# Kernel optimization log

Hardware: AMD Instinct MI355X
Metric: run time of the kernel (lower is better)

## Reference

```python
import jax, jax.numpy as jnp
import numpy as np

B, DAYS, N, E = 2, 8, 10000, 80000
C_IN, C_OUT, H = 32, 32, 4
NEG_SLOPE = 0.2


def setup_inputs() -> dict:
    key = jax.random.key(0)
    ks = jax.random.split(key, 7)
    x = jax.random.randint(ks[0], (B, DAYS, N), 0, N)
    adjacency = jax.random.randint(ks[1], (2, E), 0, N)
    embedding = jax.random.normal(ks[2], (N, C_IN), dtype=jnp.float32)
    # GATConv linear: in_channels -> heads*out_channels
    W = jax.random.normal(ks[3], (C_IN, H * C_OUT), dtype=jnp.float32) / np.sqrt(C_IN)
    att_src = jax.random.normal(ks[4], (H, C_OUT), dtype=jnp.float32) / np.sqrt(C_OUT)
    att_dst = jax.random.normal(ks[5], (H, C_OUT), dtype=jnp.float32) / np.sqrt(C_OUT)
    bias = jnp.zeros((H * C_OUT,), dtype=jnp.float32)
    return {"x": x, "adjacency": adjacency, "embedding": embedding,
            "W": W, "att_src": att_src, "att_dst": att_dst, "bias": bias}


def _gat_forward(feat, src, dst, W, att_src, att_dst, bias):
    # feat: [G, N, C_IN]; same edge list shared across the G graphs
    G = feat.shape[0]
    xh = (feat @ W).reshape(G, N, H, C_OUT)              # [G,N,H,C]
    a_src = jnp.einsum('gnhc,hc->gnh', xh, att_src)       # [G,N,H]
    a_dst = jnp.einsum('gnhc,hc->gnh', xh, att_dst)
    alpha = a_src[:, src] + a_dst[:, dst]                 # [G,Et,H]
    alpha = jnp.where(alpha >= 0, alpha, NEG_SLOPE * alpha)

    def per_graph(al, msgs):
        # segment softmax over incoming edges of each dst node
        m = jax.ops.segment_max(al, dst, num_segments=N)  # [N,H]
        e = jnp.exp(al - m[dst])                          # [Et,H]
        s = jax.ops.segment_sum(e, dst, num_segments=N)
        w = e / (s[dst] + 1e-16)
        out = jax.ops.segment_sum(w[..., None] * msgs, dst, num_segments=N)
        return out                                        # [N,H,C]

    out = jax.vmap(per_graph)(alpha, xh[:, src])          # [G,N,H,C]
    return out.reshape(G, N, H * C_OUT) + bias


def reference(x, adjacency, embedding, W, att_src, att_dst, bias):
    Bd, Dd = x.shape[0], x.shape[1]
    feat = embedding[x].reshape(-1, N, C_IN)              # [G,N,C_IN]
    # GATConv default add_self_loops=True
    loops = jnp.arange(N, dtype=adjacency.dtype)
    src = jnp.concatenate([adjacency[0], loops])
    dst = jnp.concatenate([adjacency[1], loops])
    out = _gat_forward(feat, src, dst, W, att_src, att_dst, bias)
    return out.reshape(Bd, Dd, -1)
```

## Files before the change

### kernel.cpp

```cpp
#include <hip/hip_runtime.h>
#include <hip/hip_bf16.h>
#include <math.h>

#define C_IN 32
#define H 4
#define C_OUT 32
#define HC (H * C_OUT)
#define NEG_SLOPE 0.2f
#define CSR_STRIDE 64

typedef float v2f __attribute__((ext_vector_type(2)));

#define RPB 16
__global__ __launch_bounds__(256) void build_kernel(
        const int* __restrict__ adj, int E, int N,
        int* __restrict__ deg, int* __restrict__ csr,
        const float* __restrict__ emb, const float* __restrict__ W,
        const float* __restrict__ att_src, const float* __restrict__ att_dst,
        __hip_bfloat16* __restrict__ T, float* __restrict__ ta_src,
        float* __restrict__ ta_dst, int tblocks) {
    if ((int)blockIdx.x >= tblocks) {
        int e = (blockIdx.x - tblocks) * 256 + threadIdx.x;
        int Et = E + N;
        if (e < Et) {
            int s = (e < E) ? adj[e] : (e - E);
            int d = (e < E) ? adj[E + e] : (e - E);
            int pos = atomicAdd(&deg[d], 1);
            if (pos < CSR_STRIDE) csr[(d << 6) + pos] = s;
        }
        return;
    }
    int t = threadIdx.x;
    int sub = t >> 7;
    int tc = t & 127;
    int h = tc >> 5, c = tc & 31;
    int base = blockIdx.x * RPB;
    int nmax = (N - base < RPB) ? (N - base) : RPB;

    float wcol[C_IN];
#pragma unroll
    for (int k = 0; k < C_IN; k++) wcol[k] = W[k * HC + tc];
    float as = att_src[h * C_OUT + c];
    float adw = att_dst[h * C_OUT + c];

    for (int it = sub; it < nmax; it += 2) {
        int r = __builtin_amdgcn_readfirstlane(base + it);
        const float* ep = emb + (size_t)r * C_IN;
        float acc = 0.f;
#pragma unroll
        for (int k = 0; k < C_IN; k++) acc += ep[k] * wcol[k];
        T[(size_t)r * HC + tc] = __float2bfloat16(acc);
        float ps = acc * as, pd = acc * adw;
#pragma unroll
        for (int o = 16; o; o >>= 1) {
            ps += __shfl_xor(ps, o, 32);
            pd += __shfl_xor(pd, o, 32);
        }
        if (c == 0) {
            ta_src[r * H + h] = ps;
            ta_dst[r * H + h] = pd;
        }
    }
}

__global__ __launch_bounds__(256) void agg_kernel(
        const int* __restrict__ deg, const int* __restrict__ csr,
        const int* __restrict__ x, const unsigned int* __restrict__ Tu,
        const float* __restrict__ ta_src, const float* __restrict__ ta_dst,
        const float* __restrict__ bias, float* __restrict__ out, int N, int G) {
    __shared__ float w_lds[16][CSR_STRIDE][4];
    __shared__ int   xs_lds[16][CSR_STRIDE];
    __shared__ float ds_lds[16][4];

    int t = threadIdx.x;
    int n = blockIdx.x;
    int dg = deg[n];
    if (dg > CSR_STRIDE) dg = CSR_STRIDE;
    const int* cb = csr + (n << 6);

    {
        int g = t >> 4;
        int es = (t >> 2) & 3;
        int h = t & 3;
        int xgn = x[(size_t)g * N + n];
        float adv = ta_dst[xgn * H + h];
        float dpart = 0.f;
        for (int c0 = 0; c0 < dg; c0 += 4) {
            int e = c0 + es;
            if (e < dg) {
                int s = cb[e];
                int xs = x[(size_t)g * N + s];
                float a = ta_src[xs * H + h] + adv;
                a = fmaxf(a, NEG_SLOPE * a);
                float w = __expf(a);
                w_lds[g][e][h] = w;
                dpart += w;
                if (h == 0) xs_lds[g][e] = xs;
            }
        }
        dpart += __shfl_xor(dpart, 4, 64);
        dpart += __shfl_xor(dpart, 8, 64);
        if (es == 0) ds_lds[g][h] = dpart;
    }
    __syncthreads();

    int wid = t >> 6;
    int lane = t & 63;
    int h2 = lane >> 4;
    int g0 = wid * 4;

    v2f acc[4];
#pragma unroll
    for (int j = 0; j < 4; j++) acc[j] = (v2f){0.f, 0.f};

#pragma unroll 2
    for (int e = 0; e < dg; e++) {
#pragma unroll
        for (int j = 0; j < 4; j++) {
            int xs = __builtin_amdgcn_readfirstlane(xs_lds[g0 + j][e]);
            float w = w_lds[g0 + j][e][h2];
            unsigned int u = Tu[(xs << 6) + lane];
            v2f tr = {__uint_as_float(u << 16),
                      __uint_as_float(u & 0xffff0000u)};
            acc[j] += (v2f){w, w} * tr;
        }
    }

    float2 b2 = *(const float2*)(bias + lane * 2);
    size_t obase = (size_t)n * HC + lane * 2;
#pragma unroll
    for (int j = 0; j < 4; j++) {
        int gj = g0 + j;
        float inv = __builtin_amdgcn_rcpf(ds_lds[gj][h2] + 1e-16f);
        float2 o2;
        o2.x = acc[j].x * inv + b2.x;
        o2.y = acc[j].y * inv + b2.y;
        *(float2*)(out + obase + (size_t)gj * N * HC) = o2;
    }
}

extern "C" void kernel_launch(void* const* d_in, const int* in_sizes, int n_in,
                              void* d_out, int out_size, void* d_ws, size_t ws_size,
                              hipStream_t stream) {
    const int*   x       = (const int*)d_in[0];
    const int*   adj     = (const int*)d_in[1];
    const float* emb     = (const float*)d_in[2];
    const float* W       = (const float*)d_in[3];
    const float* att_src = (const float*)d_in[4];
    const float* att_dst = (const float*)d_in[5];
    const float* bias    = (const float*)d_in[6];
    float* out = (float*)d_out;

    const int N  = in_sizes[2] / C_IN;
    const int GN = in_sizes[0];
    const int G  = GN / N;
    const int E  = in_sizes[1] / 2;
    const int Et = E + N;

    char* ws = (char*)d_ws;
    size_t o = 0;
    auto carve = [&](size_t bytes) -> void* {
        void* p = ws + o;
        o = (o + bytes + 255) & ~(size_t)255;
        return p;
    };
    __hip_bfloat16* T = (__hip_bfloat16*)carve((size_t)N * HC * sizeof(__hip_bfloat16));
    float* ta_src  = (float*)carve((size_t)N * H * sizeof(float));
    float* ta_dst  = (float*)carve((size_t)N * H * sizeof(float));
    int*   deg     = (int*)carve((size_t)N * sizeof(int));
    int*   csr     = (int*)carve((size_t)N * CSR_STRIDE * sizeof(int));

    hipMemsetAsync(deg, 0, (size_t)N * sizeof(int), stream);

    int tblocks = (N + RPB - 1) / RPB;
    int fblocks = (Et + 255) / 256;
    build_kernel<<<tblocks + fblocks, 256, 0, stream>>>(
        adj, E, N, deg, csr, emb, W, att_src, att_dst, T, ta_src, ta_dst, tblocks);

    agg_kernel<<<N, 256, 0, stream>>>(deg, csr, x,
                                      (const unsigned int*)T, ta_src, ta_dst,
                                      bias, out, N, G);
}
```

Baseline: 157.6 us.

## Give each lane group its own graph and use 16-byte gathers in aggregation

Restructures the aggregation loop so each wavefront handles four graphs at once, with 16 lanes per graph, and each lane loads 8 bf16 features as one uint4. The old scheme had each wave loop over four graphs with 4-byte loads per lane. Source offsets are pre-shifted into byte offsets, and the weight LDS array is transposed to edge-major order. Output is written as two float4 stores per lane. This cuts the number of gather instructions per edge and drops readfirstlane, at the cost of divergent per-group addresses within a wave.

```diff
diff --git a/kernel.cpp b/kernel.cpp
--- a/kernel.cpp
+++ b/kernel.cpp
@@ -68,8 +68,8 @@
         const int* __restrict__ x, const unsigned int* __restrict__ Tu,
         const float* __restrict__ ta_src, const float* __restrict__ ta_dst,
         const float* __restrict__ bias, float* __restrict__ out, int N, int G) {
-    __shared__ float w_lds[16][CSR_STRIDE][4];
-    __shared__ int   xs_lds[16][CSR_STRIDE];
+    __shared__ float w_lds[CSR_STRIDE][16][4];
+    __shared__ int   xs8_lds[16][65];
     __shared__ float ds_lds[16][4];
 
     int t = threadIdx.x;
@@ -93,9 +93,9 @@
                 float a = ta_src[xs * H + h] + adv;
                 a = fmaxf(a, NEG_SLOPE * a);
                 float w = __expf(a);
-                w_lds[g][e][h] = w;
+                w_lds[e][g][h] = w;
                 dpart += w;
-                if (h == 0) xs_lds[g][e] = xs;
+                if (h == 0) xs8_lds[g][e] = xs << 8;
             }
         }
         dpart += __shfl_xor(dpart, 4, 64);
@@ -106,37 +106,39 @@
 
     int wid = t >> 6;
     int lane = t & 63;
-    int h2 = lane >> 4;
-    int g0 = wid * 4;
+    int lg = lane >> 4;
+    int li = lane & 15;
+    int gj = wid * 4 + lg;
+    int hh = li >> 2;
+    int li16 = li << 4;
 
-    v2f acc[4];
-#pragma unroll
-    for (int j = 0; j < 4; j++) acc[j] = (v2f){0.f, 0.f};
+    v2f a0 = {0.f, 0.f}, a1 = {0.f, 0.f}, a2 = {0.f, 0.f}, a3 = {0.f, 0.f};
 
 #pragma unroll 2
     for (int e = 0; e < dg; e++) {
-#pragma unroll
-        for (int j = 0; j < 4; j++) {
-            int xs = __builtin_amdgcn_readfirstlane(xs_lds[g0 + j][e]);
-            float w = w_lds[g0 + j][e][h2];
-            unsigned int u = Tu[(xs << 6) + lane];
-            v2f tr = {__uint_as_float(u << 16),
-                      __uint_as_float(u & 0xffff0000u)};
-            acc[j] += (v2f){w, w} * tr;
-        }
+        int off = xs8_lds[gj][e] + li16;
+        float w = w_lds[e][gj][hh];
+        uint4 u = *(const uint4*)((const char*)Tu + off);
+        a0.x += w * __uint_as_float(u.x << 16);
+        a0.y += w * __uint_as_float(u.x & 0xffff0000u);
+        a1.x += w * __uint_as_float(u.y << 16);
+        a1.y += w * __uint_as_float(u.y & 0xffff0000u);
+        a2.x += w * __uint_as_float(u.z << 16);
+        a2.y += w * __uint_as_float(u.z & 0xffff0000u);
+        a3.x += w * __uint_as_float(u.w << 16);
+        a3.y += w * __uint_as_float(u.w & 0xffff0000u);
     }
 
-    float2 b2 = *(const float2*)(bias + lane * 2);
-    size_t obase = (size_t)n * HC + lane * 2;
-#pragma unroll
-    for (int j = 0; j < 4; j++) {
-        int gj = g0 + j;
-        float inv = __builtin_amdgcn_rcpf(ds_lds[gj][h2] + 1e-16f);
-        float2 o2;
-        o2.x = acc[j].x * inv + b2.x;
-        o2.y = acc[j].y * inv + b2.y;
-        *(float2*)(out + obase + (size_t)gj * N * HC) = o2;
-    }
+    float inv = __builtin_amdgcn_rcpf(ds_lds[gj][hh] + 1e-16f);
+    const float4* bp = (const float4*)(bias + li * 8);
+    float4 b0 = bp[0], b1 = bp[1];
+    float4 o0 = {a0.x * inv + b0.x, a0.y * inv + b0.y,
+                 a1.x * inv + b0.z, a1.y * inv + b0.w};
+    float4 o1 = {a2.x * inv + b1.x, a2.y * inv + b1.y,
+                 a3.x * inv + b1.z, a3.y * inv + b1.w};
+    float* op = out + (size_t)gj * N * HC + (size_t)n * HC + li * 8;
+    *(float4*)op = o0;
+    *(float4*)(op + 4) = o1;
 }
 
 extern "C" void kernel_launch(void* const* d_in, const int* in_sizes, int n_in,
```

Result: faster. 150.2 us (-4.7%).
